# Kernel optimization log

Measured on AMD Instinct MI355X. Metric: run time of the kernel, lower is better.

The kernel has to match this reference:

```python
import math
import jax, jax.numpy as jnp
import numpy as np

D_MODEL = 512
HEAD = 8
D_K = D_MODEL // HEAD
N_BUCKETS = 128
ROUNDS = 4
BIG = 1000000000.0


def look_back(x, zeros=True):
    # x: [b, n_chunks, chunk, ...] -> [b, n_chunks, 2*chunk, ...]
    pad_shape = (x.shape[0], 1) + x.shape[2:]
    if zeros:
        pad = jnp.zeros(pad_shape, x.dtype)
    else:
        pad = jnp.full(pad_shape, 1000000000, x.dtype)
    p = jnp.concatenate([pad, x], axis=1)
    return jnp.concatenate([p[:, :-1], p[:, 1:]], axis=2)


def setup_inputs() -> dict:
    key = jax.random.key(0)
    ks = jax.random.split(key, 8)
    B, L = 2, 4096
    query = jax.random.normal(ks[0], (B, L, D_MODEL), jnp.float32)
    value = jax.random.normal(ks[1], (B, L, D_MODEL), jnp.float32)
    mask = jnp.ones((B, L), dtype=bool)
    s = 1.0 / math.sqrt(D_MODEL)
    Wq = jax.random.normal(ks[2], (D_MODEL, D_MODEL), jnp.float32) * s
    bq = jnp.zeros((D_MODEL,), jnp.float32)
    Wv = jax.random.normal(ks[3], (D_MODEL, D_MODEL), jnp.float32) * s
    bv = jnp.zeros((D_MODEL,), jnp.float32)
    Wo = jax.random.normal(ks[4], (D_MODEL, D_MODEL), jnp.float32) * s
    bo = jnp.zeros((D_MODEL,), jnp.float32)
    # random LSH projection (module draws it per call; fixed here for determinism)
    rand_matrix = jax.random.uniform(ks[5], (D_K, ROUNDS, N_BUCKETS // 2), jnp.float32)
    return {"query": query, "value": value, "mask": mask, "Wq": Wq, "bq": bq,
            "Wv": Wv, "bv": bv, "Wo": Wo, "bo": bo, "rand_matrix": rand_matrix}


def lsh_attention(q, v, mask, rand_matrix):
    b, head, L, d_k = q.shape
    bh = b * head
    nb2 = N_BUCKETS // 2
    bl = L // N_BUCKETS
    R = ROUNDS
    # normalize queries, hash them
    q = q / jnp.linalg.norm(q, axis=-1, keepdims=True)
    fq = q.reshape(bh, L, d_k)
    rm = rand_matrix / jnp.linalg.norm(rand_matrix, axis=-1, keepdims=True)
    proj = jnp.einsum('bli,irk->blrk', fq, rm)                 # [bh,L,R,nb2]
    hashes = jnp.argmax(jnp.concatenate([proj, -proj], axis=-1), axis=-1)  # [bh,L,R]
    hash_indices = jnp.argsort(hashes, axis=1)                 # sorted order per round
    sorted_hashes = jnp.take_along_axis(hashes, hash_indices, axis=1)
    # gather queries into sorted order, chunk into buckets of 2*bl
    idx_qd = jnp.broadcast_to(hash_indices[:, :, None, :], (bh, L, d_k, R))
    rq = jnp.take_along_axis(jnp.broadcast_to(fq[:, :, :, None], (bh, L, d_k, R)), idx_qd, axis=1)
    rq = rq.reshape(bh, nb2, 2 * bl, d_k, R)
    lbk = look_back(rq)                                        # [bh,nb2,4bl,d_k,R]
    scores = jnp.einsum('bcidr,bcjdr->bcijr', rq, lbk) / math.sqrt(d_k)
    scores = scores.reshape(bh, L, 4 * bl, R)
    # padding mask
    m = jnp.broadcast_to(mask[:, None, :, None], (b, head, L, R)).reshape(bh, L, R)
    rmask = jnp.take_along_axis(m, hash_indices, axis=1).reshape(bh, nb2, 2 * bl, R)
    lbm = look_back(rmask, zeros=True)                         # pad -> False
    fm = jnp.broadcast_to(lbm[:, :, None, :, :], (bh, nb2, 2 * bl, 4 * bl, R)).reshape(bh, L, 4 * bl, R)
    scores = scores - (~fm).astype(scores.dtype) * BIG
    # same-hash mask
    sh = sorted_hashes.reshape(bh, nb2, 2 * bl, R)
    lbh = look_back(sh, zeros=False)
    heq = (sh[:, :, :, None, :] == lbh[:, :, None, :, :]).reshape(bh, L, 4 * bl, R)
    scores = scores - (~heq).astype(scores.dtype) * BIG
    # causal + self masks on original positions
    qi = hash_indices.reshape(bh, nb2, 2 * bl, R)
    ki = look_back(qi, zeros=False)
    causal = (qi[:, :, :, None, :] < ki[:, :, None, :, :]).reshape(bh, L, 4 * bl, R)
    scores = scores - causal.astype(scores.dtype) * BIG
    ieq = (qi[:, :, :, None, :] == ki[:, :, None, :, :]).reshape(bh, L, 4 * bl, R)
    scores = scores - ieq.astype(scores.dtype) * 100000.0
    # scatter scores back to original query order, correct duplicate keys across rounds
    original_indices = jnp.argsort(hash_indices, axis=1)
    score_indices = jnp.broadcast_to(original_indices[:, :, None, :], (bh, L, 4 * bl, R))
    fki = jnp.broadcast_to(ki[:, :, None, :, :], (bh, nb2, 2 * bl, 4 * bl, R)).reshape(bh, L, 4 * bl, R)
    rki = jnp.take_along_axis(fki, score_indices, axis=1)
    counts = [jnp.ones(rki.shape[:-1], jnp.int32) for _ in range(R)]
    for i in range(R - 1):
        for j in range(R - 1 - i):  # faithfully mirrors original indexing (incl. its j-offset)
            comp = (rki[..., i] == rki[..., i + 1 + j]).astype(jnp.int32)
            counts[i] = counts[i] + comp
            counts[j] = counts[j] + comp
    count_repeat_key = jnp.stack(counts, axis=-1)
    scores = jnp.take_along_axis(scores, score_indices, axis=1)
    scores = scores - jnp.log(count_repeat_key.astype(scores.dtype))
    p_attn = jax.nn.softmax(scores.reshape(bh, L, 4 * bl * R), axis=-1)
    # gather values into sorted order
    fv = v.reshape(bh, L, d_k)
    rv = jnp.take_along_axis(jnp.broadcast_to(fv[:, :, :, None], (bh, L, d_k, R)), idx_qd, axis=1)
    rv = rv.reshape(bh, nb2, 2 * bl, d_k, R)
    lbv = look_back(rv)                                        # [bh,nb2,4bl,d_k,R]
    attn_indices = jnp.broadcast_to(hash_indices[:, :, None, :], (bh, L, 4 * bl, R)).reshape(bh, L, 4 * bl * R)
    rp = jnp.take_along_axis(p_attn, attn_indices, axis=1).reshape(bh, nb2, 2 * bl, 4 * bl, R)
    out = jnp.einsum('bcikr,bckdr->bcidr', rp, lbv).reshape(bh, L, d_k, R)
    oi = jnp.broadcast_to(original_indices[:, :, None, :], (bh, L, d_k, R))
    out = jnp.take_along_axis(out, oi, axis=1).sum(axis=-1)
    return out.reshape(b, head, L, d_k)


def reference(query, value, mask, Wq, bq, Wv, bv, Wo, bo, rand_matrix):
    B, L, _ = query.shape
    q = (query @ Wq.T + bq).reshape(B, L, HEAD, D_K).transpose(0, 2, 1, 3)
    v = (value @ Wv.T + bv).reshape(B, L, HEAD, D_K).transpose(0, 2, 1, 3)
    x = lsh_attention(q, v, mask, rand_matrix)
    x = x.transpose(0, 2, 1, 3).reshape(B, L, HEAD * D_K)
    return x @ Wo.T + bo
```

## Files before the change

### kernel.cpp

```cpp
#include <hip/hip_runtime.h>

#define L4   4096
#define DK   64
#define NR   4
#define NB   128
#define WIN  128
#define DM   512
#define BH   16
#define BIGF 1000000000.0f

typedef short v8s __attribute__((ext_vector_type(8)));
typedef float v4f __attribute__((ext_vector_type(4)));

__device__ __forceinline__ unsigned short f2bf(float x) {
  union { float f; unsigned u; } v; v.f = x;
  const unsigned r = (v.u + 0x7FFFu + ((v.u >> 16) & 1u)) >> 16;
  return (unsigned short)r;
}
__device__ __forceinline__ float bf2f(unsigned short u) {
  union { unsigned u; float f; } v; v.u = ((unsigned)u) << 16;
  return v.f;
}
__device__ __forceinline__ ushort4 f2bf4(const float4 x) {
  ushort4 r; r.x = f2bf(x.x); r.y = f2bf(x.y); r.z = f2bf(x.z); r.w = f2bf(x.w);
  return r;
}

__device__ float g_fqn[(size_t)BH * L4 * DK];
__device__ unsigned short g_fqb[(size_t)BH * L4 * DK];
__device__ unsigned short g_fvb[(size_t)BH * L4 * DK];
__device__ float g_rmnT[NR * 64 * DK];
__device__ int   g_hash [BH * NR * L4];
__device__ int   g_sidx [BH * NR * L4];
__device__ int   g_shash[BH * NR * L4];
__device__ int   g_inv  [BH * NR * L4];
__device__ unsigned char g_cnt[(size_t)BH * NR * L4 * WIN];
__device__ float2 g_stat[BH * NR * L4];
__device__ float2 g_MZ  [BH * L4];
__device__ unsigned short g_p[(size_t)BH * NR * L4 * WIN];
__device__ unsigned short g_osortb[(size_t)BH * NR * L4 * DK];
__device__ unsigned short g_xb[(size_t)2 * L4 * DM];

__global__ __launch_bounds__(256) void stage1_kernel(const float* __restrict__ A,
                                                     const float* __restrict__ Wq,
                                                     const float* __restrict__ bq,
                                                     const float* __restrict__ Vf,
                                                     const float* __restrict__ Wv,
                                                     const float* __restrict__ bv,
                                                     const float* __restrict__ rm)
{
  __shared__ __align__(16) char smem[27648];
  const int bid = blockIdx.x;
  const int tid = threadIdx.x;
  if (bid < 512) {
    float (*As)[132] = (float(*)[132])smem;
    float (*Bs)[68]  = (float(*)[68])(smem + 16896);
    const int m0 = (bid & 63) * 128;
    const int n0 = (bid >> 6) * 64;
    const int am = tid & 127, ak0 = (tid >> 7) * 16;
    const int bn = tid & 63,  bk0 = (tid >> 6) * 8;
    const float* arow = A + (size_t)(m0 + am) * DM + ak0;
    const float* brow = Wq + (size_t)(n0 + bn) * DM + bk0;
    float4 pa0 = *(const float4*)(arow);
    float4 pa1 = *(const float4*)(arow + 4);
    float4 pa2 = *(const float4*)(arow + 8);
    float4 pa3 = *(const float4*)(arow + 12);
    float4 pb0 = *(const float4*)(brow);
    float4 pb1 = *(const float4*)(brow + 4);
    const int lane = tid & 63, w = tid >> 6;
    const int ng = lane & 15, mgl = lane >> 4;
    const int mbase = (w * 4 + mgl) * 8;
    const int nbase = ng * 4;
    float acc[8][4] = {};
    for (int kt = 0; kt < DM; kt += 32) {
      __syncthreads();
      As[ak0 +  0][am] = pa0.x; As[ak0 +  1][am] = pa0.y; As[ak0 +  2][am] = pa0.z; As[ak0 +  3][am] = pa0.w;
      As[ak0 +  4][am] = pa1.x; As[ak0 +  5][am] = pa1.y; As[ak0 +  6][am] = pa1.z; As[ak0 +  7][am] = pa1.w;
      As[ak0 +  8][am] = pa2.x; As[ak0 +  9][am] = pa2.y; As[ak0 + 10][am] = pa2.z; As[ak0 + 11][am] = pa2.w;
      As[ak0 + 12][am] = pa3.x; As[ak0 + 13][am] = pa3.y; As[ak0 + 14][am] = pa3.z; As[ak0 + 15][am] = pa3.w;
      Bs[bk0 + 0][bn] = pb0.x; Bs[bk0 + 1][bn] = pb0.y; Bs[bk0 + 2][bn] = pb0.z; Bs[bk0 + 3][bn] = pb0.w;
      Bs[bk0 + 4][bn] = pb1.x; Bs[bk0 + 5][bn] = pb1.y; Bs[bk0 + 6][bn] = pb1.z; Bs[bk0 + 7][bn] = pb1.w;
      __syncthreads();
      if (kt + 32 < DM) {
        pa0 = *(const float4*)(arow + kt + 32);
        pa1 = *(const float4*)(arow + kt + 36);
        pa2 = *(const float4*)(arow + kt + 40);
        pa3 = *(const float4*)(arow + kt + 44);
        pb0 = *(const float4*)(brow + kt + 32);
        pb1 = *(const float4*)(brow + kt + 36);
      }
      #pragma unroll
      for (int kk = 0; kk < 32; ++kk) {
        const float4 a0 = *(const float4*)&As[kk][mbase];
        const float4 a1 = *(const float4*)&As[kk][mbase + 4];
        const float4 bv4 = *(const float4*)&Bs[kk][nbase];
        const float amv[8] = {a0.x, a0.y, a0.z, a0.w, a1.x, a1.y, a1.z, a1.w};
        const float bnv[4] = {bv4.x, bv4.y, bv4.z, bv4.w};
        #pragma unroll
        for (int i = 0; i < 8; ++i)
          #pragma unroll
          for (int j = 0; j < 4; ++j)
            acc[i][j] = fmaf(amv[i], bnv[j], acc[i][j]);
      }
    }
    #pragma unroll
    for (int j = 0; j < 4; ++j) {
      const float bb = bq[n0 + nbase + j];
      #pragma unroll
      for (int i = 0; i < 8; ++i) acc[i][j] += bb;
    }
    float sc[8];
    #pragma unroll
    for (int i = 0; i < 8; ++i) {
      float s = acc[i][0] * acc[i][0];
      s = fmaf(acc[i][1], acc[i][1], s);
      s = fmaf(acc[i][2], acc[i][2], s);
      s = fmaf(acc[i][3], acc[i][3], s);
      s += __shfl_xor(s, 1);
      s += __shfl_xor(s, 2);
      s += __shfl_xor(s, 4);
      s += __shfl_xor(s, 8);
      sc[i] = 1.0f / sqrtf(s);
    }
    const int bh = (m0 >> 12) * 8 + (n0 >> 6);
    const int lb = (m0 & (L4 - 1)) + mbase;
    #pragma unroll
    for (int i = 0; i < 8; ++i) {
      const size_t idx = ((size_t)bh * L4 + lb + i) * DK + nbase;
      float4 o;
      o.x = acc[i][0] * sc[i]; o.y = acc[i][1] * sc[i];
      o.z = acc[i][2] * sc[i]; o.w = acc[i][3] * sc[i];
      *(float4*)(g_fqn + idx) = o;
      *(ushort4*)(g_fqb + idx) = f2bf4(o);
    }
  } else if (bid < 1024) {
    unsigned short (*As)[72] = (unsigned short(*)[72])smem;
    unsigned short (*Bs)[72] = (unsigned short(*)[72])(smem + 18432);
    const int b2 = bid - 512;
    const int m0 = (b2 & 63) * 128;
    const int n0 = (b2 >> 6) * 64;
    const int lane = tid & 63, w = tid >> 6;
    const int li = lane & 15, lq = lane >> 4;
    v4f acc[2][4];
    #pragma unroll
    for (int mt = 0; mt < 2; ++mt)
      #pragma unroll
      for (int jt = 0; jt < 4; ++jt) acc[mt][jt] = (v4f){0.f, 0.f, 0.f, 0.f};
    for (int kt = 0; kt < DM; kt += 64) {
      __syncthreads();
      {
        const int row = tid >> 1, h = tid & 1;
        const float* src = Vf + (size_t)(m0 + row) * DM + kt + h * 32;
        #pragma unroll
        for (int u = 0; u < 4; ++u) {
          const float4 x = *(const float4*)(src + u * 8);
          const float4 y = *(const float4*)(src + u * 8 + 4);
          *(ushort4*)&As[row][h * 32 + u * 8]     = f2bf4(x);
          *(ushort4*)&As[row][h * 32 + u * 8 + 4] = f2bf4(y);
        }
      }
      {
        const int row = tid >> 2, p = tid & 3;
        const float* src = Wv + (size_t)(n0 + row) * DM + kt + p * 16;
        #pragma unroll
        for (int u = 0; u < 2; ++u) {
          const float4 x = *(const float4*)(src + u * 8);
          const float4 y = *(const float4*)(src + u * 8 + 4);
          *(ushort4*)&Bs[row][p * 16 + u * 8]     = f2bf4(x);
          *(ushort4*)&Bs[row][p * 16 + u * 8 + 4] = f2bf4(y);
        }
      }
      __syncthreads();
      #pragma unroll
      for (int ks = 0; ks < 2; ++ks) {
        const v8s aq0 = *(const v8s*)&As[w * 32 + li][ks * 32 + lq * 8];
        const v8s aq1 = *(const v8s*)&As[w * 32 + 16 + li][ks * 32 + lq * 8];
        #pragma unroll
        for (int jt = 0; jt < 4; ++jt) {
          const v8s bk = *(const v8s*)&Bs[jt * 16 + li][ks * 32 + lq * 8];
          acc[0][jt] = __builtin_amdgcn_mfma_f32_16x16x32_bf16(aq0, bk, acc[0][jt], 0, 0, 0);
          acc[1][jt] = __builtin_amdgcn_mfma_f32_16x16x32_bf16(aq1, bk, acc[1][jt], 0, 0, 0);
        }
      }
    }
    #pragma unroll
    for (int mt = 0; mt < 2; ++mt)
      #pragma unroll
      for (int jt = 0; jt < 4; ++jt)
        #pragma unroll
        for (int reg = 0; reg < 4; ++reg) {
          const int m = m0 + w * 32 + mt * 16 + lq * 4 + reg;
          const int n = n0 + jt * 16 + li;
          const float vv = acc[mt][jt][reg] + bv[n];
          const int bh = (m >> 12) * 8 + (n >> 6);
          const int l = m & (L4 - 1);
          g_fvb[((size_t)bh * L4 + l) * DK + (n & 63)] = f2bf(vv);
        }
  } else {
    const int dr = (bid - 1024) * 4 + (tid >> 6);
    const int k = tid & 63;
    const float v = rm[dr * 64 + k];
    float s = v * v;
    #pragma unroll
    for (int off = 32; off; off >>= 1) s += __shfl_xor(s, off);
    const int d = dr >> 2, r = dr & 3;
    g_rmnT[(r * 64 + k) * DK + d] = v / sqrtf(s);
  }
}

__global__ __launch_bounds__(256) void mgemm2(const float* __restrict__ W,
                                              const float* __restrict__ bias,
                                              float* __restrict__ outp)
{
  const int m0 = blockIdx.x * 128;
  const int n0 = blockIdx.y * 64;
  __shared__ unsigned short As[128][72];
  __shared__ unsigned short Bs[64][72];
  const int tid = threadIdx.x;
  const int lane = tid & 63, w = tid >> 6;
  const int li = lane & 15, lq = lane >> 4;
  v4f acc[2][4];
  #pragma unroll
  for (int mt = 0; mt < 2; ++mt)
    #pragma unroll
    for (int jt = 0; jt < 4; ++jt) acc[mt][jt] = (v4f){0.f, 0.f, 0.f, 0.f};
  for (int kt = 0; kt < DM; kt += 64) {
    __syncthreads();
    {
      const int row = tid >> 1, h = tid & 1;
      const unsigned short* src = g_xb + (size_t)(m0 + row) * DM + kt + h * 32;
      #pragma unroll
      for (int u = 0; u < 4; ++u)
        *(uint4*)&As[row][h * 32 + u * 8] = ((const uint4*)src)[u];
    }
    {
      const int row = tid >> 2, p = tid & 3;
      const float* src = W + (size_t)(n0 + row) * DM + kt + p * 16;
      #pragma unroll
      for (int u = 0; u < 2; ++u) {
        const float4 x = *(const float4*)(src + u * 8);
        const float4 y = *(const float4*)(src + u * 8 + 4);
        *(ushort4*)&Bs[row][p * 16 + u * 8]     = f2bf4(x);
        *(ushort4*)&Bs[row][p * 16 + u * 8 + 4] = f2bf4(y);
      }
    }
    __syncthreads();
    #pragma unroll
    for (int ks = 0; ks < 2; ++ks) {
      const v8s aq0 = *(const v8s*)&As[w * 32 + li][ks * 32 + lq * 8];
      const v8s aq1 = *(const v8s*)&As[w * 32 + 16 + li][ks * 32 + lq * 8];
      #pragma unroll
      for (int jt = 0; jt < 4; ++jt) {
        const v8s bk = *(const v8s*)&Bs[jt * 16 + li][ks * 32 + lq * 8];
        acc[0][jt] = __builtin_amdgcn_mfma_f32_16x16x32_bf16(aq0, bk, acc[0][jt], 0, 0, 0);
        acc[1][jt] = __builtin_amdgcn_mfma_f32_16x16x32_bf16(aq1, bk, acc[1][jt], 0, 0, 0);
      }
    }
  }
  #pragma unroll
  for (int mt = 0; mt < 2; ++mt)
    #pragma unroll
    for (int jt = 0; jt < 4; ++jt)
      #pragma unroll
      for (int reg = 0; reg < 4; ++reg) {
        const int m = m0 + w * 32 + mt * 16 + lq * 4 + reg;
        const int n = n0 + jt * 16 + li;
        outp[(size_t)m * DM + n] = acc[mt][jt][reg] + bias[n];
      }
}

__global__ __launch_bounds__(256, 4) void hash_kernel() {
  const int tid = threadIdx.x;
  const int w = __builtin_amdgcn_readfirstlane(tid >> 6);
  const int lane = tid & 63;
  const int row = blockIdx.x * 64 + lane;
  float q[64];
  #pragma unroll
  for (int du = 0; du < 16; ++du) {
    const float4 v = *(const float4*)(g_fqn + (size_t)row * DK + du * 4);
    q[du * 4 + 0] = v.x; q[du * 4 + 1] = v.y;
    q[du * 4 + 2] = v.z; q[du * 4 + 3] = v.w;
  }
  const float* rmw = g_rmnT + w * (64 * DK);
  float bestP = -BIGF, bestN = -BIGF;
  int idxP = 0, idxN = 0;
  for (int k = 0; k < 64; k += 2) {
    const float* rp0 = rmw + k * DK;
    const float* rp1 = rp0 + DK;
    float a0 = 0.f, a1 = 0.f;
    #pragma unroll
    for (int d = 0; d < 64; ++d) {
      a0 = fmaf(q[d], rp0[d], a0);
      a1 = fmaf(q[d], rp1[d], a1);
    }
    if (a0 > bestP)  { bestP = a0;  idxP = k; }
    if (-a0 > bestN) { bestN = -a0; idxN = k; }
    if (a1 > bestP)  { bestP = a1;  idxP = k + 1; }
    if (-a1 > bestN) { bestN = -a1; idxN = k + 1; }
  }
  const int idx = (bestP >= bestN) ? idxP : 64 + idxN;
  const int bh = row >> 12, l = row & (L4 - 1);
  g_hash[(bh * NR + w) * L4 + l] = idx;
}

__global__ __launch_bounds__(128) void sort_kernel() {
  __shared__ int chunkHist[64][NB];
  __shared__ int tot[NB];
  __shared__ int binBase[NB];
  const int bhr = blockIdx.x;
  const int t = threadIdx.x;
  const int* hrow = g_hash + bhr * L4;
  for (int idx = t; idx < 64 * NB; idx += 128) ((int*)chunkHist)[idx] = 0;
  __syncthreads();
  if (t < 64) {
    for (int e = 0; e < 64; ++e) chunkHist[t][hrow[t * 64 + e]]++;
  }
  __syncthreads();
  if (t < NB) { int s = 0; for (int cc = 0; cc < 64; ++cc) s += chunkHist[cc][t]; tot[t] = s; }
  __syncthreads();
  if (t == 0) { int run = 0; for (int h = 0; h < NB; ++h) { binBase[h] = run; run += tot[h]; } }
  __syncthreads();
  if (t < NB) {
    int run = binBase[t];
    for (int cc = 0; cc < 64; ++cc) { const int tmp = chunkHist[cc][t]; chunkHist[cc][t] = run; run += tmp; }
  }
  __syncthreads();
  if (t < 64) {
    for (int e = 0; e < 64; ++e) {
      const int l = t * 64 + e;
      const int h = hrow[l];
      const int p = chunkHist[t][h]++;
      g_sidx [bhr * L4 + p] = l;
      g_shash[bhr * L4 + p] = h;
      g_inv  [bhr * L4 + l] = p;
    }
  }
}

__global__ __launch_bounds__(256) void counts_kernel() {
  const int bh = blockIdx.x;
  const int l0 = blockIdx.y * 32;
  const int j = threadIdx.x & 127;
  const int lh = threadIdx.x >> 7;
  for (int u = 0; u < 16; ++u) {
    const int l = l0 + u * 2 + lh;
    int a[4];
    #pragma unroll
    for (int r = 0; r < NR; ++r) {
      const int base = (bh * NR + r) * L4;
      const int spos = g_inv[base + l];
      const int c = spos >> 6;
      a[r] = (c == 0 && j < 64) ? (1 << 20) : g_sidx[base + c * 64 - 64 + j];
    }
    const int c01 = a[0] == a[1], c02 = a[0] == a[2], c03 = a[0] == a[3];
    const int c12 = a[1] == a[2], c13 = a[1] == a[3], c23 = a[2] == a[3];
    const unsigned char n0 = (unsigned char)(1 + 2 * c01 + c02 + c03 + c12 + c23);
    const unsigned char n1 = (unsigned char)(1 + c02 + c12 + 2 * c13);
    const unsigned char n2 = (unsigned char)(1 + c03 + c23);
    g_cnt[((size_t)(bh * NR + 0) * L4 + l) * WIN + j] = n0;
    g_cnt[((size_t)(bh * NR + 1) * L4 + l) * WIN + j] = n1;
    g_cnt[((size_t)(bh * NR + 2) * L4 + l) * WIN + j] = n2;
  }
}

__global__ __launch_bounds__(256) void passA_kernel() {
  const int c = blockIdx.x, r = blockIdx.y, bh = blockIdx.z;
  const int base = (bh * NR + r) * L4;
  const int s0 = c * 64;
  const bool use_cnt = (r != 3);
  __shared__ unsigned short QKP[13824];
  __shared__ unsigned char cnt8[64][128];
  __shared__ int qi_s[64], qh_s[64], ki_s[128], kh_s[128];
  __shared__ float lutl[9];
  unsigned short (*Qb)[72] = (unsigned short(*)[72])QKP;
  unsigned short (*Kb)[72] = (unsigned short(*)[72])(QKP + 64 * 72);
  unsigned short (*Pt)[136] = (unsigned short(*)[136])QKP;
  const int tid = threadIdx.x;
  if (tid < 9) lutl[tid] = __logf((float)(tid < 1 ? 1 : tid));
  {
    const int i = tid >> 2, p = tid & 3;
    const int qi = g_sidx[base + s0 + i];
    if (p == 0) { qi_s[i] = qi; qh_s[i] = g_shash[base + s0 + i]; }
    const uint4* src = (const uint4*)(g_fqb + ((size_t)bh * L4 + qi) * DK);
    *(uint4*)&Qb[i][p * 16]     = src[2 * p];
    *(uint4*)&Qb[i][p * 16 + 8] = src[2 * p + 1];
    if (use_cnt) {
      const uint4* cs = (const uint4*)(g_cnt + (size_t)(base + qi) * WIN);
      *(uint4*)&cnt8[i][p * 32]      = cs[2 * p];
      *(uint4*)&cnt8[i][p * 32 + 16] = cs[2 * p + 1];
    }
  }
  {
    const int j = tid >> 1, h = tid & 1;
    const bool pad = (c == 0) && (j < 64);
    if (pad) {
      if (h == 0) { ki_s[j] = -1; kh_s[j] = (1 << 30); }
      const uint4 z = make_uint4(0, 0, 0, 0);
      #pragma unroll
      for (int u = 0; u < 4; ++u) *(uint4*)&Kb[j][h * 32 + u * 8] = z;
    } else {
      const int ki = g_sidx[base + s0 - 64 + j];
      if (h == 0) { ki_s[j] = ki; kh_s[j] = g_shash[base + s0 - 64 + j]; }
      const uint4* src = (const uint4*)(g_fqb + ((size_t)bh * L4 + ki) * DK);
      #pragma unroll
      for (int u = 0; u < 4; ++u) *(uint4*)&Kb[j][h * 32 + u * 8] = src[h * 4 + u];
    }
  }
  __syncthreads();
  const int lane = tid & 63, w = tid >> 6;
  const int i0 = w * 16;
  const int li = lane & 15, lq = lane >> 4;
  v4f acc[8];
  #pragma unroll
  for (int jt = 0; jt < 8; ++jt) acc[jt] = (v4f){0.f, 0.f, 0.f, 0.f};
  #pragma unroll
  for (int ks = 0; ks < 2; ++ks) {
    const v8s aq = *(const v8s*)&Qb[i0 + li][ks * 32 + lq * 8];
    #pragma unroll
    for (int jt = 0; jt < 8; ++jt) {
      const v8s bk = *(const v8s*)&Kb[jt * 16 + li][ks * 32 + lq * 8];
      acc[jt] = __builtin_amdgcn_mfma_f32_16x16x32_bf16(aq, bk, acc[jt], 0, 0, 0);
    }
  }
  float mrow[4], zrow[4];
  #pragma unroll
  for (int reg = 0; reg < 4; ++reg) {
    const int i = i0 + lq * 4 + reg;
    const int qi = qi_s[i], qh = qh_s[i];
    float lm = -3.0f * BIGF;
    #pragma unroll
    for (int jt = 0; jt < 8; ++jt) {
      const int j = jt * 16 + li;
      const int ki = ki_s[j], kh = kh_s[j];
      float s;
      if (ki < 0) {
        s = 0.f - BIGF - BIGF - BIGF;
      } else {
        s = acc[jt][reg] * 0.125f;
        if (qh != kh) s -= BIGF;
        if (qi < ki)  s -= BIGF;
        if (qi == ki) s -= 100000.0f;
        if (use_cnt) s -= lutl[cnt8[i][j]];
      }
      acc[jt][reg] = s;
      lm = fmaxf(lm, s);
    }
    #pragma unroll
    for (int off = 1; off < 16; off <<= 1) lm = fmaxf(lm, __shfl_xor(lm, off));
    mrow[reg] = lm;
    float ps = 0.f;
    #pragma unroll
    for (int jt = 0; jt < 8; ++jt) ps += __expf(acc[jt][reg] - lm);
    #pragma unroll
    for (int off = 1; off < 16; off <<= 1) ps += __shfl_xor(ps, off);
    zrow[reg] = ps;
    if (li == 0) g_stat[base + s0 + i] = make_float2(lm, ps);
  }
  __syncthreads();
  #pragma unroll
  for (int reg = 0; reg < 4; ++reg) {
    const int i = i0 + lq * 4 + reg;
    #pragma unroll
    for (int jt = 0; jt < 8; ++jt)
      Pt[i][jt * 16 + li] = f2bf(__expf(acc[jt][reg] - mrow[reg]));
  }
  __syncthreads();
  unsigned short* gp = g_p + ((size_t)(base + s0)) * WIN;
  #pragma unroll
  for (int it = 0; it < 4; ++it) {
    const int t = tid + it * 256;
    const int row = t >> 4, colu = t & 15;
    ((uint4*)gp)[t] = *(const uint4*)&Pt[row][colu * 8];
  }
}

__global__ __launch_bounds__(256) void merge_kernel() {
  const int idx = blockIdx.x * 256 + threadIdx.x;
  const int bh = idx >> 12, l = idx & (L4 - 1);
  float m[4], z[4];
  #pragma unroll
  for (int r = 0; r < NR; ++r) {
    const int base = (bh * NR + r) * L4;
    const int spos = g_inv[base + l];
    const float2 st = g_stat[base + spos];
    m[r] = st.x; z[r] = st.y;
  }
  const float M = fmaxf(fmaxf(m[0], m[1]), fmaxf(m[2], m[3]));
  const float Z = z[0] * __expf(m[0] - M) + z[1] * __expf(m[1] - M)
                + z[2] * __expf(m[2] - M) + z[3] * __expf(m[3] - M);
  g_MZ[idx] = make_float2(M, 1.0f / Z);
}

__global__ __launch_bounds__(256) void passB_kernel() {
  const int c = blockIdx.x, r = blockIdx.y, bh = blockIdx.z;
  const int base = (bh * NR + r) * L4;
  const int s0 = c * 64;
  __shared__ unsigned short Pb[64][136];
  __shared__ unsigned short Vt[64][136];
  __shared__ float scale_s[64];
  const int tid = threadIdx.x;
  const unsigned short* gp = g_p + ((size_t)(base + s0)) * WIN;
  #pragma unroll
  for (int it = 0; it < 4; ++it) {
    const int t = tid + it * 256;
    const int row = t >> 4, colu = t & 15;
    *(uint4*)&Pb[row][colu * 8] = ((const uint4*)gp)[t];
  }
  if (tid < 64) {
    const float m_r = g_stat[base + s0 + tid].x;
    const int qi = g_sidx[base + s0 + tid];
    const float2 mz = g_MZ[(size_t)bh * L4 + qi];
    scale_s[tid] = __expf(m_r - mz.x) * mz.y;
  }
  {
    const int j = tid >> 1, h = tid & 1;
    const bool pad = (c == 0) && (j < 64);
    if (pad) {
      #pragma unroll
      for (int d = 0; d < 32; ++d) Vt[h * 32 + d][j] = 0;
    } else {
      const int ki = g_sidx[base + s0 - 64 + j];
      const uint4* src = (const uint4*)(g_fvb + ((size_t)bh * L4 + ki) * DK);
      #pragma unroll
      for (int u = 0; u < 4; ++u) {
        const uint4 v = src[h * 4 + u];
        const unsigned short* e = (const unsigned short*)&v;
        #pragma unroll
        for (int t = 0; t < 8; ++t) Vt[h * 32 + u * 8 + t][j] = e[t];
      }
    }
  }
  __syncthreads();
  const int lane = tid & 63, w = tid >> 6;
  const int i0 = w * 16;
  const int li = lane & 15, lq = lane >> 4;
  v4f acc[4];
  #pragma unroll
  for (int dt = 0; dt < 4; ++dt) acc[dt] = (v4f){0.f, 0.f, 0.f, 0.f};
  #pragma unroll
  for (int ks = 0; ks < 4; ++ks) {
    const v8s pa = *(const v8s*)&Pb[i0 + li][ks * 32 + lq * 8];
    #pragma unroll
    for (int dt = 0; dt < 4; ++dt) {
      const v8s vb = *(const v8s*)&Vt[dt * 16 + li][ks * 32 + lq * 8];
      acc[dt] = __builtin_amdgcn_mfma_f32_16x16x32_bf16(pa, vb, acc[dt], 0, 0, 0);
    }
  }
  #pragma unroll
  for (int reg = 0; reg < 4; ++reg) {
    const int i = i0 + lq * 4 + reg;
    const float sc = scale_s[i];
    unsigned short* orow = g_osortb + ((size_t)(base + s0 + i)) * DK;
    #pragma unroll
    for (int dt = 0; dt < 4; ++dt)
      orow[dt * 16 + li] = f2bf(acc[dt][reg] * sc);
  }
}

__global__ __launch_bounds__(256) void combine_kernel() {
  const int b = blockIdx.x >> 12, l = blockIdx.x & (L4 - 1);
  const int tid = threadIdx.x;
  const int d = tid & 63, h0 = tid >> 6;
  #pragma unroll
  for (int hh = h0; hh < 8; hh += 4) {
    const int bh = b * 8 + hh;
    float v = 0.f;
    #pragma unroll
    for (int r = 0; r < NR; ++r) {
      const int s = g_inv[(bh * NR + r) * L4 + l];
      v += bf2f(g_osortb[((size_t)(bh * NR + r) * L4 + s) * DK + d]);
    }
    g_xb[((size_t)b * L4 + l) * DM + hh * 64 + d] = f2bf(v);
  }
}

extern "C" void kernel_launch(void* const* d_in, const int* in_sizes, int n_in,
                              void* d_out, int out_size, void* d_ws, size_t ws_size,
                              hipStream_t stream) {
  (void)in_sizes; (void)n_in; (void)d_ws; (void)ws_size; (void)out_size;
  const float* query = (const float*)d_in[0];
  const float* value = (const float*)d_in[1];
  const float* Wq = (const float*)d_in[3];
  const float* bq = (const float*)d_in[4];
  const float* Wv = (const float*)d_in[5];
  const float* bv = (const float*)d_in[6];
  const float* Wo = (const float*)d_in[7];
  const float* bo = (const float*)d_in[8];
  const float* rm = (const float*)d_in[9];
  float* out = (float*)d_out;

  stage1_kernel<<<1088, 256, 0, stream>>>(query, Wq, bq, value, Wv, bv, rm);
  hash_kernel<<<1024, 256, 0, stream>>>();
  sort_kernel<<<64, 128, 0, stream>>>();
  counts_kernel<<<dim3(16, 128), 256, 0, stream>>>();
  passA_kernel<<<dim3(64, 4, 16), 256, 0, stream>>>();
  merge_kernel<<<256, 256, 0, stream>>>();
  passB_kernel<<<dim3(64, 4, 16), 256, 0, stream>>>();
  combine_kernel<<<8192, 256, 0, stream>>>();
  mgemm2<<<dim3(64, 8), 256, 0, stream>>>(Wo, bo, out);
}
```

Measured before the change: 283.2 us.

## Fuse LSH hashing into Q projection epilogue via shared memory

Moves the hash computation into the Q-projection GEMM blocks. Each block stages its normalized fp32 query tile in shared memory and computes the bucket argmax for its rows there, so the fp32 normalized-query buffer no longer has to be written to and read back from global memory. The random-matrix normalization becomes its own small kernel that runs first, because the fused epilogue reads its output. The cost is more shared memory per block, which can lower occupancy, and extra serial work in the 512 Q-GEMM blocks while the V-GEMM blocks finish sooner.

```diff
diff --git a/kernel.cpp b/kernel.cpp
--- a/kernel.cpp
+++ b/kernel.cpp
@@ -26,7 +26,6 @@
   return r;
 }
 
-__device__ float g_fqn[(size_t)BH * L4 * DK];
 __device__ unsigned short g_fqb[(size_t)BH * L4 * DK];
 __device__ unsigned short g_fvb[(size_t)BH * L4 * DK];
 __device__ float g_rmnT[NR * 64 * DK];
@@ -41,20 +40,31 @@
 __device__ unsigned short g_osortb[(size_t)BH * NR * L4 * DK];
 __device__ unsigned short g_xb[(size_t)2 * L4 * DM];
 
+__global__ __launch_bounds__(64) void rmnorm_kernel(const float* __restrict__ rm) {
+  const int dr = blockIdx.x;
+  const int k = threadIdx.x;
+  const float v = rm[dr * 64 + k];
+  float s = v * v;
+  #pragma unroll
+  for (int off = 32; off; off >>= 1) s += __shfl_xor(s, off);
+  const int d = dr >> 2, r = dr & 3;
+  g_rmnT[(r * 64 + k) * DK + d] = v / sqrtf(s);
+}
+
 __global__ __launch_bounds__(256) void stage1_kernel(const float* __restrict__ A,
                                                      const float* __restrict__ Wq,
                                                      const float* __restrict__ bq,
                                                      const float* __restrict__ Vf,
                                                      const float* __restrict__ Wv,
-                                                     const float* __restrict__ bv,
-                                                     const float* __restrict__ rm)
+                                                     const float* __restrict__ bv)
 {
-  __shared__ __align__(16) char smem[27648];
+  __shared__ __align__(16) char smem[34816];
   const int bid = blockIdx.x;
   const int tid = threadIdx.x;
   if (bid < 512) {
     float (*As)[132] = (float(*)[132])smem;
     float (*Bs)[68]  = (float(*)[68])(smem + 16896);
+    float (*qs)[68]  = (float(*)[68])smem;
     const int m0 = (bid & 63) * 128;
     const int n0 = (bid >> 6) * 64;
     const int am = tid & 127, ak0 = (tid >> 7) * 16;
@@ -124,16 +134,50 @@
     }
     const int bh = (m0 >> 12) * 8 + (n0 >> 6);
     const int lb = (m0 & (L4 - 1)) + mbase;
+    __syncthreads();
     #pragma unroll
     for (int i = 0; i < 8; ++i) {
       const size_t idx = ((size_t)bh * L4 + lb + i) * DK + nbase;
       float4 o;
       o.x = acc[i][0] * sc[i]; o.y = acc[i][1] * sc[i];
       o.z = acc[i][2] * sc[i]; o.w = acc[i][3] * sc[i];
-      *(float4*)(g_fqn + idx) = o;
       *(ushort4*)(g_fqb + idx) = f2bf4(o);
-    }
-  } else if (bid < 1024) {
+      *(float4*)&qs[mbase + i][nbase] = o;
+    }
+    __syncthreads();
+    const int w4 = __builtin_amdgcn_readfirstlane(tid >> 6);
+    const float* rmw = g_rmnT + w4 * (64 * DK);
+    const int lbase = m0 & (L4 - 1);
+    #pragma unroll
+    for (int half = 0; half < 2; ++half) {
+      const int rr = half * 64 + lane;
+      float q[64];
+      #pragma unroll
+      for (int du = 0; du < 16; ++du) {
+        const float4 v = *(const float4*)&qs[rr][du * 4];
+        q[du * 4 + 0] = v.x; q[du * 4 + 1] = v.y;
+        q[du * 4 + 2] = v.z; q[du * 4 + 3] = v.w;
+      }
+      float bestP = -BIGF, bestN = -BIGF;
+      int idxP = 0, idxN = 0;
+      for (int k = 0; k < 64; k += 2) {
+        const float* rp0 = rmw + k * DK;
+        const float* rp1 = rp0 + DK;
+        float a0 = 0.f, a1 = 0.f;
+        #pragma unroll
+        for (int d = 0; d < 64; ++d) {
+          a0 = fmaf(q[d], rp0[d], a0);
+          a1 = fmaf(q[d], rp1[d], a1);
+        }
+        if (a0 > bestP)  { bestP = a0;  idxP = k; }
+        if (-a0 > bestN) { bestN = -a0; idxN = k; }
+        if (a1 > bestP)  { bestP = a1;  idxP = k + 1; }
+        if (-a1 > bestN) { bestN = -a1; idxN = k + 1; }
+      }
+      const int hidx = (bestP >= bestN) ? idxP : 64 + idxN;
+      g_hash[(bh * NR + w4) * L4 + lbase + rr] = hidx;
+    }
+  } else {
     unsigned short (*As)[72] = (unsigned short(*)[72])smem;
     unsigned short (*Bs)[72] = (unsigned short(*)[72])(smem + 18432);
     const int b2 = bid - 512;
@@ -196,15 +240,6 @@
           const int l = m & (L4 - 1);
           g_fvb[((size_t)bh * L4 + l) * DK + (n & 63)] = f2bf(vv);
         }
-  } else {
-    const int dr = (bid - 1024) * 4 + (tid >> 6);
-    const int k = tid & 63;
-    const float v = rm[dr * 64 + k];
-    float s = v * v;
-    #pragma unroll
-    for (int off = 32; off; off >>= 1) s += __shfl_xor(s, off);
-    const int d = dr >> 2, r = dr & 3;
-    g_rmnT[(r * 64 + k) * DK + d] = v / sqrtf(s);
   }
 }
 
@@ -267,40 +302,6 @@
         const int n = n0 + jt * 16 + li;
         outp[(size_t)m * DM + n] = acc[mt][jt][reg] + bias[n];
       }
-}
-
-__global__ __launch_bounds__(256, 4) void hash_kernel() {
-  const int tid = threadIdx.x;
-  const int w = __builtin_amdgcn_readfirstlane(tid >> 6);
-  const int lane = tid & 63;
-  const int row = blockIdx.x * 64 + lane;
-  float q[64];
-  #pragma unroll
-  for (int du = 0; du < 16; ++du) {
-    const float4 v = *(const float4*)(g_fqn + (size_t)row * DK + du * 4);
-    q[du * 4 + 0] = v.x; q[du * 4 + 1] = v.y;
-    q[du * 4 + 2] = v.z; q[du * 4 + 3] = v.w;
-  }
-  const float* rmw = g_rmnT + w * (64 * DK);
-  float bestP = -BIGF, bestN = -BIGF;
-  int idxP = 0, idxN = 0;
-  for (int k = 0; k < 64; k += 2) {
-    const float* rp0 = rmw + k * DK;
-    const float* rp1 = rp0 + DK;
-    float a0 = 0.f, a1 = 0.f;
-    #pragma unroll
-    for (int d = 0; d < 64; ++d) {
-      a0 = fmaf(q[d], rp0[d], a0);
-      a1 = fmaf(q[d], rp1[d], a1);
-    }
-    if (a0 > bestP)  { bestP = a0;  idxP = k; }
-    if (-a0 > bestN) { bestN = -a0; idxN = k; }
-    if (a1 > bestP)  { bestP = a1;  idxP = k + 1; }
-    if (-a1 > bestN) { bestN = -a1; idxN = k + 1; }
-  }
-  const int idx = (bestP >= bestN) ? idxP : 64 + idxN;
-  const int bh = row >> 12, l = row & (L4 - 1);
-  g_hash[(bh * NR + w) * L4 + l] = idx;
 }
 
 __global__ __launch_bounds__(128) void sort_kernel() {
@@ -589,8 +590,8 @@
   const float* rm = (const float*)d_in[9];
   float* out = (float*)d_out;
 
-  stage1_kernel<<<1088, 256, 0, stream>>>(query, Wq, bq, value, Wv, bv, rm);
-  hash_kernel<<<1024, 256, 0, stream>>>();
+  rmnorm_kernel<<<256, 64, 0, stream>>>(rm);
+  stage1_kernel<<<1024, 256, 0, stream>>>(query, Wq, bq, value, Wv, bv);
   sort_kernel<<<64, 128, 0, stream>>>();
   counts_kernel<<<dim3(16, 128), 256, 0, stream>>>();
   passA_kernel<<<dim3(64, 4, 16), 256, 0, stream>>>();
```

New measurement: 343.2 us. 21.2% more time.

## Fuse P·V into passA and apply softmax rescale in combine

Applied to the files above, without the earlier changes.

The P·V matmul moves into passA, which now keeps the unnormalized probabilities in shared memory and writes unscaled outputs. The global P buffer and the separate passB launch are removed. The cross-round normalization (exp(m_r - M)/Z) moves into combine_kernel, which reads per-row stats. This avoids writing and rereading a large bf16 probability tensor, at the cost of more shared memory in passA and extra gathered reads in combine.

```diff
diff --git a/kernel.cpp b/kernel.cpp
--- a/kernel.cpp
+++ b/kernel.cpp
@@ -37,7 +37,6 @@
 __device__ unsigned char g_cnt[(size_t)BH * NR * L4 * WIN];
 __device__ float2 g_stat[BH * NR * L4];
 __device__ float2 g_MZ  [BH * L4];
-__device__ unsigned short g_p[(size_t)BH * NR * L4 * WIN];
 __device__ unsigned short g_osortb[(size_t)BH * NR * L4 * DK];
 __device__ unsigned short g_xb[(size_t)2 * L4 * DM];
 
@@ -208,67 +207,6 @@
   }
 }
 
-__global__ __launch_bounds__(256) void mgemm2(const float* __restrict__ W,
-                                              const float* __restrict__ bias,
-                                              float* __restrict__ outp)
-{
-  const int m0 = blockIdx.x * 128;
-  const int n0 = blockIdx.y * 64;
-  __shared__ unsigned short As[128][72];
-  __shared__ unsigned short Bs[64][72];
-  const int tid = threadIdx.x;
-  const int lane = tid & 63, w = tid >> 6;
-  const int li = lane & 15, lq = lane >> 4;
-  v4f acc[2][4];
-  #pragma unroll
-  for (int mt = 0; mt < 2; ++mt)
-    #pragma unroll
-    for (int jt = 0; jt < 4; ++jt) acc[mt][jt] = (v4f){0.f, 0.f, 0.f, 0.f};
-  for (int kt = 0; kt < DM; kt += 64) {
-    __syncthreads();
-    {
-      const int row = tid >> 1, h = tid & 1;
-      const unsigned short* src = g_xb + (size_t)(m0 + row) * DM + kt + h * 32;
-      #pragma unroll
-      for (int u = 0; u < 4; ++u)
-        *(uint4*)&As[row][h * 32 + u * 8] = ((const uint4*)src)[u];
-    }
-    {
-      const int row = tid >> 2, p = tid & 3;
-      const float* src = W + (size_t)(n0 + row) * DM + kt + p * 16;
-      #pragma unroll
-      for (int u = 0; u < 2; ++u) {
-        const float4 x = *(const float4*)(src + u * 8);
-        const float4 y = *(const float4*)(src + u * 8 + 4);
-        *(ushort4*)&Bs[row][p * 16 + u * 8]     = f2bf4(x);
-        *(ushort4*)&Bs[row][p * 16 + u * 8 + 4] = f2bf4(y);
-      }
-    }
-    __syncthreads();
-    #pragma unroll
-    for (int ks = 0; ks < 2; ++ks) {
-      const v8s aq0 = *(const v8s*)&As[w * 32 + li][ks * 32 + lq * 8];
-      const v8s aq1 = *(const v8s*)&As[w * 32 + 16 + li][ks * 32 + lq * 8];
-      #pragma unroll
-      for (int jt = 0; jt < 4; ++jt) {
-        const v8s bk = *(const v8s*)&Bs[jt * 16 + li][ks * 32 + lq * 8];
-        acc[0][jt] = __builtin_amdgcn_mfma_f32_16x16x32_bf16(aq0, bk, acc[0][jt], 0, 0, 0);
-        acc[1][jt] = __builtin_amdgcn_mfma_f32_16x16x32_bf16(aq1, bk, acc[1][jt], 0, 0, 0);
-      }
-    }
-  }
-  #pragma unroll
-  for (int mt = 0; mt < 2; ++mt)
-    #pragma unroll
-    for (int jt = 0; jt < 4; ++jt)
-      #pragma unroll
-      for (int reg = 0; reg < 4; ++reg) {
-        const int m = m0 + w * 32 + mt * 16 + lq * 4 + reg;
-        const int n = n0 + jt * 16 + li;
-        outp[(size_t)m * DM + n] = acc[mt][jt][reg] + bias[n];
-      }
-}
-
 __global__ __launch_bounds__(256, 4) void hash_kernel() {
   const int tid = threadIdx.x;
   const int w = __builtin_amdgcn_readfirstlane(tid >> 6);
@@ -368,13 +306,14 @@
   const int base = (bh * NR + r) * L4;
   const int s0 = c * 64;
   const bool use_cnt = (r != 3);
-  __shared__ unsigned short QKP[13824];
-  __shared__ unsigned char cnt8[64][128];
+  __shared__ __align__(16) char smem[35840];
+  unsigned short (*Qb)[72] = (unsigned short(*)[72])smem;
+  unsigned short (*Kb)[72] = (unsigned short(*)[72])(smem + 9216);
+  unsigned char (*cnt8)[128] = (unsigned char(*)[128])(smem + 27648);
+  unsigned short (*Pt)[136] = (unsigned short(*)[136])smem;
+  unsigned short (*Vt)[136] = (unsigned short(*)[136])(smem + 17408);
   __shared__ int qi_s[64], qh_s[64], ki_s[128], kh_s[128];
   __shared__ float lutl[9];
-  unsigned short (*Qb)[72] = (unsigned short(*)[72])QKP;
-  unsigned short (*Kb)[72] = (unsigned short(*)[72])(QKP + 64 * 72);
-  unsigned short (*Pt)[136] = (unsigned short(*)[136])QKP;
   const int tid = threadIdx.x;
   if (tid < 9) lutl[tid] = __logf((float)(tid < 1 ? 1 : tid));
   {
@@ -422,7 +361,7 @@
       acc[jt] = __builtin_amdgcn_mfma_f32_16x16x32_bf16(aq, bk, acc[jt], 0, 0, 0);
     }
   }
-  float mrow[4], zrow[4];
+  float mrow[4];
   #pragma unroll
   for (int reg = 0; reg < 4; ++reg) {
     const int i = i0 + lq * 4 + reg;
@@ -453,7 +392,6 @@
     for (int jt = 0; jt < 8; ++jt) ps += __expf(acc[jt][reg] - lm);
     #pragma unroll
     for (int off = 1; off < 16; off <<= 1) ps += __shfl_xor(ps, off);
-    zrow[reg] = ps;
     if (li == 0) g_stat[base + s0 + i] = make_float2(lm, ps);
   }
   __syncthreads();
@@ -464,13 +402,44 @@
     for (int jt = 0; jt < 8; ++jt)
       Pt[i][jt * 16 + li] = f2bf(__expf(acc[jt][reg] - mrow[reg]));
   }
-  __syncthreads();
-  unsigned short* gp = g_p + ((size_t)(base + s0)) * WIN;
-  #pragma unroll
-  for (int it = 0; it < 4; ++it) {
-    const int t = tid + it * 256;
-    const int row = t >> 4, colu = t & 15;
-    ((uint4*)gp)[t] = *(const uint4*)&Pt[row][colu * 8];
+  {
+    const int j = tid >> 1, h = tid & 1;
+    const bool pad = (c == 0) && (j < 64);
+    if (pad) {
+      #pragma unroll
+      for (int d = 0; d < 32; ++d) Vt[h * 32 + d][j] = 0;
+    } else {
+      const int ki = g_sidx[base + s0 - 64 + j];
+      const uint4* src = (const uint4*)(g_fvb + ((size_t)bh * L4 + ki) * DK);
+      #pragma unroll
+      for (int u = 0; u < 4; ++u) {
+        const uint4 v = src[h * 4 + u];
+        const unsigned short* e = (const unsigned short*)&v;
+        #pragma unroll
+        for (int t = 0; t < 8; ++t) Vt[h * 32 + u * 8 + t][j] = e[t];
+      }
+    }
+  }
+  __syncthreads();
+  v4f acc2[4];
+  #pragma unroll
+  for (int dt = 0; dt < 4; ++dt) acc2[dt] = (v4f){0.f, 0.f, 0.f, 0.f};
+  #pragma unroll
+  for (int ks = 0; ks < 4; ++ks) {
+    const v8s pa = *(const v8s*)&Pt[i0 + li][ks * 32 + lq * 8];
+    #pragma unroll
+    for (int dt = 0; dt < 4; ++dt) {
+      const v8s vb = *(const v8s*)&Vt[dt * 16 + li][ks * 32 + lq * 8];
+      acc2[dt] = __builtin_amdgcn_mfma_f32_16x16x32_bf16(pa, vb, acc2[dt], 0, 0, 0);
+    }
+  }
+  #pragma unroll
+  for (int reg = 0; reg < 4; ++reg) {
+    const int i = i0 + lq * 4 + reg;
+    unsigned short* orow = g_osortb + ((size_t)(base + s0 + i)) * DK;
+    #pragma unroll
+    for (int dt = 0; dt < 4; ++dt)
+      orow[dt * 16 + li] = f2bf(acc2[dt][reg]);
   }
 }
 
@@ -491,72 +460,6 @@
   g_MZ[idx] = make_float2(M, 1.0f / Z);
 }
 
-__global__ __launch_bounds__(256) void passB_kernel() {
-  const int c = blockIdx.x, r = blockIdx.y, bh = blockIdx.z;
-  const int base = (bh * NR + r) * L4;
-  const int s0 = c * 64;
-  __shared__ unsigned short Pb[64][136];
-  __shared__ unsigned short Vt[64][136];
-  __shared__ float scale_s[64];
-  const int tid = threadIdx.x;
-  const unsigned short* gp = g_p + ((size_t)(base + s0)) * WIN;
-  #pragma unroll
-  for (int it = 0; it < 4; ++it) {
-    const int t = tid + it * 256;
-    const int row = t >> 4, colu = t & 15;
-    *(uint4*)&Pb[row][colu * 8] = ((const uint4*)gp)[t];
-  }
-  if (tid < 64) {
-    const float m_r = g_stat[base + s0 + tid].x;
-    const int qi = g_sidx[base + s0 + tid];
-    const float2 mz = g_MZ[(size_t)bh * L4 + qi];
-    scale_s[tid] = __expf(m_r - mz.x) * mz.y;
-  }
-  {
-    const int j = tid >> 1, h = tid & 1;
-    const bool pad = (c == 0) && (j < 64);
-    if (pad) {
-      #pragma unroll
-      for (int d = 0; d < 32; ++d) Vt[h * 32 + d][j] = 0;
-    } else {
-      const int ki = g_sidx[base + s0 - 64 + j];
-      const uint4* src = (const uint4*)(g_fvb + ((size_t)bh * L4 + ki) * DK);
-      #pragma unroll
-      for (int u = 0; u < 4; ++u) {
-        const uint4 v = src[h * 4 + u];
-        const unsigned short* e = (const unsigned short*)&v;
-        #pragma unroll
-        for (int t = 0; t < 8; ++t) Vt[h * 32 + u * 8 + t][j] = e[t];
-      }
-    }
-  }
-  __syncthreads();
-  const int lane = tid & 63, w = tid >> 6;
-  const int i0 = w * 16;
-  const int li = lane & 15, lq = lane >> 4;
-  v4f acc[4];
-  #pragma unroll
-  for (int dt = 0; dt < 4; ++dt) acc[dt] = (v4f){0.f, 0.f, 0.f, 0.f};
-  #pragma unroll
-  for (int ks = 0; ks < 4; ++ks) {
-    const v8s pa = *(const v8s*)&Pb[i0 + li][ks * 32 + lq * 8];
-    #pragma unroll
-    for (int dt = 0; dt < 4; ++dt) {
-      const v8s vb = *(const v8s*)&Vt[dt * 16 + li][ks * 32 + lq * 8];
-      acc[dt] = __builtin_amdgcn_mfma_f32_16x16x32_bf16(pa, vb, acc[dt], 0, 0, 0);
-    }
-  }
-  #pragma unroll
-  for (int reg = 0; reg < 4; ++reg) {
-    const int i = i0 + lq * 4 + reg;
-    const float sc = scale_s[i];
-    unsigned short* orow = g_osortb + ((size_t)(base + s0 + i)) * DK;
-    #pragma unroll
-    for (int dt = 0; dt < 4; ++dt)
-      orow[dt * 16 + li] = f2bf(acc[dt][reg] * sc);
-  }
-}
-
 __global__ __launch_bounds__(256) void combine_kernel() {
   const int b = blockIdx.x >> 12, l = blockIdx.x & (L4 - 1);
   const int tid = threadIdx.x;
@@ -564,14 +467,79 @@
   #pragma unroll
   for (int hh = h0; hh < 8; hh += 4) {
     const int bh = b * 8 + hh;
+    const float2 mz = g_MZ[(size_t)bh * L4 + l];
     float v = 0.f;
     #pragma unroll
     for (int r = 0; r < NR; ++r) {
-      const int s = g_inv[(bh * NR + r) * L4 + l];
-      v += bf2f(g_osortb[((size_t)(bh * NR + r) * L4 + s) * DK + d]);
+      const int base = (bh * NR + r) * L4;
+      const int s = g_inv[base + l];
+      const float m_r = g_stat[base + s].x;
+      const float scale = __expf(m_r - mz.x) * mz.y;
+      v += bf2f(g_osortb[((size_t)base + s) * DK + d]) * scale;
     }
     g_xb[((size_t)b * L4 + l) * DM + hh * 64 + d] = f2bf(v);
   }
+}
+
+__global__ __launch_bounds__(256) void mgemm2(const float* __restrict__ W,
+                                              const float* __restrict__ bias,
+                                              float* __restrict__ outp)
+{
+  const int m0 = blockIdx.x * 128;
+  const int n0 = blockIdx.y * 64;
+  __shared__ unsigned short As[128][72];
+  __shared__ unsigned short Bs[64][72];
+  const int tid = threadIdx.x;
+  const int lane = tid & 63, w = tid >> 6;
+  const int li = lane & 15, lq = lane >> 4;
+  v4f acc[2][4];
+  #pragma unroll
+  for (int mt = 0; mt < 2; ++mt)
+    #pragma unroll
+    for (int jt = 0; jt < 4; ++jt) acc[mt][jt] = (v4f){0.f, 0.f, 0.f, 0.f};
+  for (int kt = 0; kt < DM; kt += 64) {
+    __syncthreads();
+    {
+      const int row = tid >> 1, h = tid & 1;
+      const unsigned short* src = g_xb + (size_t)(m0 + row) * DM + kt + h * 32;
+      #pragma unroll
+      for (int u = 0; u < 4; ++u)
+        *(uint4*)&As[row][h * 32 + u * 8] = ((const uint4*)src)[u];
+    }
+    {
+      const int row = tid >> 2, p = tid & 3;
+      const float* src = W + (size_t)(n0 + row) * DM + kt + p * 16;
+      #pragma unroll
+      for (int u = 0; u < 2; ++u) {
+        const float4 x = *(const float4*)(src + u * 8);
+        const float4 y = *(const float4*)(src + u * 8 + 4);
+        *(ushort4*)&Bs[row][p * 16 + u * 8]     = f2bf4(x);
+        *(ushort4*)&Bs[row][p * 16 + u * 8 + 4] = f2bf4(y);
+      }
+    }
+    __syncthreads();
+    #pragma unroll
+    for (int ks = 0; ks < 2; ++ks) {
+      const v8s aq0 = *(const v8s*)&As[w * 32 + li][ks * 32 + lq * 8];
+      const v8s aq1 = *(const v8s*)&As[w * 32 + 16 + li][ks * 32 + lq * 8];
+      #pragma unroll
+      for (int jt = 0; jt < 4; ++jt) {
+        const v8s bk = *(const v8s*)&Bs[jt * 16 + li][ks * 32 + lq * 8];
+        acc[0][jt] = __builtin_amdgcn_mfma_f32_16x16x32_bf16(aq0, bk, acc[0][jt], 0, 0, 0);
+        acc[1][jt] = __builtin_amdgcn_mfma_f32_16x16x32_bf16(aq1, bk, acc[1][jt], 0, 0, 0);
+      }
+    }
+  }
+  #pragma unroll
+  for (int mt = 0; mt < 2; ++mt)
+    #pragma unroll
+    for (int jt = 0; jt < 4; ++jt)
+      #pragma unroll
+      for (int reg = 0; reg < 4; ++reg) {
+        const int m = m0 + w * 32 + mt * 16 + lq * 4 + reg;
+        const int n = n0 + jt * 16 + li;
+        outp[(size_t)m * DM + n] = acc[mt][jt][reg] + bias[n];
+      }
 }
 
 extern "C" void kernel_launch(void* const* d_in, const int* in_sizes, int n_in,
@@ -595,7 +563,6 @@
   counts_kernel<<<dim3(16, 128), 256, 0, stream>>>();
   passA_kernel<<<dim3(64, 4, 16), 256, 0, stream>>>();
   merge_kernel<<<256, 256, 0, stream>>>();
-  passB_kernel<<<dim3(64, 4, 16), 256, 0, stream>>>();
   combine_kernel<<<8192, 256, 0, stream>>>();
   mgemm2<<<dim3(64, 8), 256, 0, stream>>>(Wo, bo, out);
 }
```

New measurement: 266.7 us. 5.8% less time.
